# Kernel tuning notes

Measured on AMD Instinct MI355X. Metric: run time of the kernel, lower is better.

## Reference

```python
import jax, jax.numpy as jnp
import numpy as np

N, H, L, O = 8192, 512, 3, 512
LN_EPS = 1e-5


def setup_inputs() -> dict:
    key = jax.random.key(0)
    ks = jax.random.split(key, 8)
    # sparse symmetric adjacency with positive weights, zero diagonal
    u = jax.random.uniform(ks[0], (N, N))
    w = jax.random.uniform(ks[1], (N, N)) * 0.9 + 0.1
    A = jnp.where(u < 0.004, w, 0.0)
    A = (A + A.T) * 0.5
    A = A * (1.0 - jnp.eye(N, dtype=A.dtype))
    s = 0.02
    return {
        "node_feat": jax.random.normal(ks[2], (1, N, H), jnp.float32),
        "adj": A[None],
        "conv_w": jax.random.normal(ks[3], (L, H, H), jnp.float32) * s,
        "conv_b": jnp.zeros((L, H), jnp.float32),
        "mlp_w": jax.random.normal(ks[4], (L, H, H), jnp.float32) * s,
        "mlp_b": jnp.zeros((L, H), jnp.float32),
        "ln_g": jnp.ones((L, H), jnp.float32),
        "ln_b": jnp.zeros((L, H), jnp.float32),
        "lin_w": jax.random.normal(ks[5], (H, O), jnp.float32) * s,
        "lin_b": jnp.zeros((O,), jnp.float32),
    }


def _layer_norm(x, g, b):
    mu = jnp.mean(x, axis=-1, keepdims=True)
    var = jnp.mean(jnp.square(x - mu), axis=-1, keepdims=True)
    return (x - mu) * jax.lax.rsqrt(var + LN_EPS) * g + b


def reference(node_feat, adj, conv_w, conv_b, mlp_w, mlp_b, ln_g, ln_b, lin_w, lin_b):
    x = node_feat[0]          # [N, H]
    A = adj[0]                # [N, N]
    A = jnp.where(A > 0, A, 0.0)  # edges are positive entries only
    # gcn_norm: add self-loops (weight 1) only where missing
    d = jnp.diagonal(A)
    A1 = A + jnp.diag(jnp.where(d > 0, 0.0, 1.0))
    # deg scattered at target (edge_index[1] = column)
    deg = jnp.sum(A1, axis=0)
    dinv = jnp.where(deg > 0, deg ** -0.5, 0.0)
    Ahat = dinv[:, None] * A1 * dinv[None, :]  # [N, N]
    for l in range(L):
        # GCNConv: linear, propagate (aggregate at col), bias
        x = Ahat.T @ (x @ conv_w[l]) + conv_b[l]
        # MLP: Linear -> LayerNorm -> ReLU
        x = jax.nn.relu(_layer_norm(x @ mlp_w[l] + mlp_b[l], ln_g[l], ln_b[l]))
    mu = (x @ lin_w + lin_b)[None]  # [1, N, O]
    return mu
```

## Files before the change

### kernel.cpp

```cpp
#include <hip/hip_runtime.h>

#define NN 8192
#define HD 512
#define NL 3
#define CAP 128
#define LN_EPS 1e-5f

typedef _Float16 f16;
typedef _Float16 f16x8 __attribute__((ext_vector_type(8)));
typedef _Float16 f16x4 __attribute__((ext_vector_type(4)));
typedef _Float16 f16x2 __attribute__((ext_vector_type(2)));
typedef float f32x4 __attribute__((ext_vector_type(4)));

__device__ __forceinline__ unsigned short f16_bits(f16 h) {
  union { f16 h; unsigned short u; } x; x.h = h; return x.u;
}
__device__ __forceinline__ f16 bits_f16(unsigned short u) {
  union { unsigned short u; f16 h; } x; x.u = u; return x.h;
}

__global__ __launch_bounds__(256) void k_prep(const float* __restrict__ A,
                                              const float* __restrict__ x0,
                                              unsigned* __restrict__ ell,
                                              int* __restrict__ nnz8,
                                              float* __restrict__ dinv,
                                              f16* __restrict__ xs) {
  __shared__ int wtot[4];
  __shared__ float wsum[4];
  __shared__ float sdinv;
  const int r = blockIdx.x;
  const int t = threadIdx.x;
  const int lane = t & 63;
  const int wv = t >> 6;
  const float4* ar = (const float4*)(A + (size_t)r * NN);
  unsigned* er = ell + (size_t)r * CAP;

  float4 v[8];
  int c = 0;
  float s = 0.f;
  #pragma unroll
  for (int i = 0; i < 8; i++) {
    v[i] = ar[t + i * 256];
    c += (v[i].x > 0.f) + (v[i].y > 0.f) + (v[i].z > 0.f) + (v[i].w > 0.f);
    s += v[i].x + v[i].y + v[i].z + v[i].w;
  }
  int inc = c;
  #pragma unroll
  for (int d = 1; d < 64; d <<= 1) {
    int vv = __shfl_up(inc, d);
    if (lane >= d) inc += vv;
  }
  float ss = s;
  #pragma unroll
  for (int m = 1; m < 64; m <<= 1) ss += __shfl_xor(ss, m);
  if (lane == 63) wtot[wv] = inc;
  if (lane == 0) wsum[wv] = ss;
  __syncthreads();
  int base = inc - c;
  for (int w = 0; w < wv; w++) base += wtot[w];

  int o = base;
  #pragma unroll
  for (int i = 0; i < 8; i++) {
    float vals[4] = {v[i].x, v[i].y, v[i].z, v[i].w};
    #pragma unroll
    for (int q = 0; q < 4; q++) {
      float val = vals[q];
      if (val > 0.f) {
        if (o < CAP) er[o] = ((unsigned)f16_bits((f16)val) << 16) | (unsigned)((t + i * 256) * 4 + q);
        o++;
      }
    }
  }
  if (t == 255) {
    int ne = wtot[0] + wtot[1] + wtot[2] + wtot[3];
    if (ne < CAP) er[ne] = (0x3C00u << 16) | (unsigned)r;
    int ne1 = ne + 1; if (ne1 > CAP) ne1 = CAP;
    int n8 = (ne1 + 7) & ~7;
    for (int k = ne1; k < n8; k++) er[k] = (unsigned)r;
    nnz8[r] = n8;
    float deg = wsum[0] + wsum[1] + wsum[2] + wsum[3] + 1.f;
    float di = rsqrtf(deg);
    dinv[r] = di;
    sdinv = di;
  }
  __syncthreads();
  {
    const float di = sdinv;
    const float2 xv = ((const float2*)(x0 + (size_t)r * HD))[t];
    f16x2 o2 = {(f16)(xv.x * di), (f16)(xv.y * di)};
    ((f16x2*)(xs + (size_t)r * HD))[t] = o2;
  }
}

__global__ __launch_bounds__(256) void k_spmm(const unsigned* __restrict__ ell,
                                              const int* __restrict__ nnz8,
                                              const float* __restrict__ dinv,
                                              const f16* __restrict__ xs,
                                              f16* __restrict__ y) {
  const int bid = blockIdx.x;
  const int chunk = bid >> 11;
  const int rb = bid & 2047;
  const int r = __builtin_amdgcn_readfirstlane(rb * 4 + (threadIdx.x >> 6));
  const int lane = threadIdx.x & 63;
  const int c0 = chunk * 128 + lane * 2;
  const uint4* er = (const uint4*)(ell + (size_t)r * CAP);
  const int ne = nnz8[r];
  const f16* xc = xs + c0;
  float a0 = 0.f, a1 = 0.f;
  for (int e8 = 0; e8 < (ne >> 3); e8++) {
    const uint4 ea = er[e8 * 2];
    const uint4 eb = er[e8 * 2 + 1];
    unsigned wv[8] = {ea.x, ea.y, ea.z, ea.w, eb.x, eb.y, eb.z, eb.w};
    f16x2 xv[8];
    #pragma unroll
    for (int q = 0; q < 8; q++)
      xv[q] = *(const f16x2*)(xc + (size_t)(wv[q] & 0xFFFFu) * HD);
    #pragma unroll
    for (int q = 0; q < 8; q++) {
      const float fw = (float)bits_f16((unsigned short)(wv[q] >> 16));
      a0 = fmaf(fw, (float)xv[q][0], a0);
      a1 = fmaf(fw, (float)xv[q][1], a1);
    }
  }
  const float s = dinv[r];
  f16x2 o = {(f16)(a0 * s), (f16)(a1 * s)};
  *(f16x2*)(y + (size_t)r * HD + c0) = o;
}

__global__ __launch_bounds__(512) void k_gemm_ln(const f16* __restrict__ y,
                                                 const f16* __restrict__ WT,
                                                 const float* __restrict__ bias,
                                                 const float* __restrict__ g,
                                                 const float* __restrict__ bb,
                                                 const float* __restrict__ dscale,
                                                 f16* __restrict__ outp) {
  __shared__ float red[32][4][2];
  const int t = threadIdx.x;
  const int lane = t & 63;
  const int w = t >> 6;
  const int wm = w >> 2;
  const int wn = w & 3;
  const int m0 = blockIdx.x * 32;
  const int rl = lane & 15, kg = (lane >> 4) * 8;
  const f16* aP = y + (size_t)(m0 + wm * 16 + rl) * HD + kg;
  const f16* bP = WT + (size_t)(wn * 128 + rl) * HD + kg;

  f32x4 acc[8];
  #pragma unroll
  for (int j = 0; j < 8; j++) { f32x4 z = {0.f, 0.f, 0.f, 0.f}; acc[j] = z; }

  #pragma unroll 2
  for (int ks = 0; ks < HD; ks += 32) {
    const f16x8 af = *(const f16x8*)(aP + ks);
    #pragma unroll
    for (int j = 0; j < 8; j++) {
      const f16x8 bf = *(const f16x8*)(bP + (size_t)j * 16 * HD + ks);
      acc[j] = __builtin_amdgcn_mfma_f32_16x16x32_f16(af, bf, acc[j], 0, 0, 0);
    }
  }

  const int cg = lane >> 4, cl = lane & 15;
  float av[8][4];
  #pragma unroll
  for (int j = 0; j < 8; j++) {
    const float bv = bias[wn * 128 + j * 16 + cl];
    #pragma unroll
    for (int r = 0; r < 4; r++) av[j][r] = acc[j][r] + bv;
  }
  #pragma unroll
  for (int r = 0; r < 4; r++) {
    float s = 0.f, sq = 0.f;
    #pragma unroll
    for (int j = 0; j < 8; j++) { s += av[j][r]; sq += av[j][r] * av[j][r]; }
    #pragma unroll
    for (int m = 1; m < 16; m <<= 1) { s += __shfl_xor(s, m); sq += __shfl_xor(sq, m); }
    if (cl == 0) {
      red[wm * 16 + cg * 4 + r][wn][0] = s;
      red[wm * 16 + cg * 4 + r][wn][1] = sq;
    }
  }
  __syncthreads();
  #pragma unroll
  for (int r = 0; r < 4; r++) {
    const int rb = wm * 16 + cg * 4 + r;
    float s = 0.f, sq = 0.f;
    #pragma unroll
    for (int q = 0; q < 4; q++) { s += red[rb][q][0]; sq += red[rb][q][1]; }
    const float mu = s * (1.f / HD);
    const float rs = rsqrtf(sq * (1.f / HD) - mu * mu + LN_EPS);
    const int row = m0 + rb;
    const float dsc = dscale ? dscale[row] : 1.f;
    #pragma unroll
    for (int j = 0; j < 8; j++) {
      const int col = wn * 128 + j * 16 + cl;
      const float val = fmaxf((av[j][r] - mu) * rs * g[col] + bb[col], 0.f) * dsc;
      outp[(size_t)row * HD + col] = (f16)val;
    }
  }
}

__global__ __launch_bounds__(256) void k_gemm_direct(const f16* __restrict__ A,
                                                     const f16* __restrict__ BT,
                                                     float* __restrict__ C,
                                                     const float* __restrict__ bias) {
  const int t = threadIdx.x;
  const int lane = t & 63;
  const int wave = t >> 6;
  const int wm = wave >> 1, wn = wave & 1;
  const int m0 = blockIdx.x * 128, n0 = blockIdx.y * 128;
  const int rl = lane & 15, kg = (lane >> 4) * 8;

  const f16* aP[4];
  const f16* bP[4];
  #pragma unroll
  for (int i = 0; i < 4; i++)
    aP[i] = A + (size_t)(m0 + wm * 64 + i * 16 + rl) * HD + kg;
  #pragma unroll
  for (int j = 0; j < 4; j++)
    bP[j] = BT + (size_t)(n0 + wn * 64 + j * 16 + rl) * HD + kg;

  f32x4 acc[4][4];
  #pragma unroll
  for (int i = 0; i < 4; i++)
    #pragma unroll
    for (int j = 0; j < 4; j++) {
      f32x4 z = {0.f, 0.f, 0.f, 0.f};
      acc[i][j] = z;
    }

  #pragma unroll 4
  for (int ks = 0; ks < HD; ks += 32) {
    f16x8 af[4], bf[4];
    #pragma unroll
    for (int i = 0; i < 4; i++) af[i] = *(const f16x8*)(aP[i] + ks);
    #pragma unroll
    for (int j = 0; j < 4; j++) bf[j] = *(const f16x8*)(bP[j] + ks);
    #pragma unroll
    for (int i = 0; i < 4; i++)
      #pragma unroll
      for (int j = 0; j < 4; j++)
        acc[i][j] = __builtin_amdgcn_mfma_f32_16x16x32_f16(af[i], bf[j], acc[i][j], 0, 0, 0);
  }

  const int cg = lane >> 4, cl = lane & 15;
  #pragma unroll
  for (int i = 0; i < 4; i++) {
    #pragma unroll
    for (int j = 0; j < 4; j++) {
      const int col = n0 + wn * 64 + j * 16 + cl;
      const float bv = bias ? bias[col] : 0.f;
      #pragma unroll
      for (int rr = 0; rr < 4; rr++) {
        const int row = m0 + wm * 64 + i * 16 + cg * 4 + rr;
        C[(size_t)row * HD + col] = acc[i][j][rr] + bv;
      }
    }
  }
}

__global__ __launch_bounds__(256) void k_weights(const float* __restrict__ convw,
                                                 const float* __restrict__ mlpw,
                                                 const float* __restrict__ convb,
                                                 const float* __restrict__ mlpb,
                                                 const float* __restrict__ lw,
                                                 f16* __restrict__ WlT,
                                                 float* __restrict__ bl,
                                                 f16* __restrict__ lwT) {
  const int l = blockIdx.y;
  const int bx = blockIdx.x;
  const int t = threadIdx.x;
  if (bx < 256) {
    const int m0 = bx * 2;
    const float* Wc = convw + (size_t)l * HD * HD;
    const float* Wm = mlpw + (size_t)l * HD * HD;
    f16* o = WlT + (size_t)l * HD * HD;
    float a00 = 0.f, a01 = 0.f, a10 = 0.f, a11 = 0.f;
    const float* wc0 = Wc + (size_t)m0 * HD;
    const float* wc1 = Wc + (size_t)(m0 + 1) * HD;
    for (int k = 0; k < HD; k++) {
      const float w0 = Wm[(size_t)k * HD + t];
      const float w1 = Wm[(size_t)k * HD + t + 256];
      const float c0 = wc0[k];
      const float c1 = wc1[k];
      a00 = fmaf(c0, w0, a00);
      a01 = fmaf(c0, w1, a01);
      a10 = fmaf(c1, w0, a10);
      a11 = fmaf(c1, w1, a11);
    }
    o[(size_t)t * HD + m0] = (f16)a00;
    o[(size_t)(t + 256) * HD + m0] = (f16)a01;
    o[(size_t)t * HD + m0 + 1] = (f16)a10;
    o[(size_t)(t + 256) * HD + m0 + 1] = (f16)a11;
  } else if (bx == 256) {
    const float* Wm = mlpw + (size_t)l * HD * HD;
    float acc0 = mlpb[l * HD + t];
    float acc1 = mlpb[l * HD + t + 256];
    for (int k = 0; k < HD; k++) {
      const float cb = convb[l * HD + k];
      acc0 = fmaf(cb, Wm[(size_t)k * HD + t], acc0);
      acc1 = fmaf(cb, Wm[(size_t)k * HD + t + 256], acc1);
    }
    bl[l * HD + t] = acc0;
    bl[l * HD + t + 256] = acc1;
  } else if (l == 0) {
    const int base = (bx - 257) * 16384;
    #pragma unroll 4
    for (int j = 0; j < 64; j++) {
      const int idx = base + j * 256 + t;
      const int k = idx >> 9, n = idx & 511;
      lwT[(size_t)n * HD + k] = (f16)lw[idx];
    }
  }
}

extern "C" void kernel_launch(void* const* d_in, const int* in_sizes, int n_in,
                              void* d_out, int out_size, void* d_ws, size_t ws_size,
                              hipStream_t stream) {
  const float* node_feat = (const float*)d_in[0];
  const float* adj       = (const float*)d_in[1];
  const float* conv_w    = (const float*)d_in[2];
  const float* conv_b    = (const float*)d_in[3];
  const float* mlp_w     = (const float*)d_in[4];
  const float* mlp_b     = (const float*)d_in[5];
  const float* ln_g      = (const float*)d_in[6];
  const float* ln_b      = (const float*)d_in[7];
  const float* lin_w     = (const float*)d_in[8];
  const float* lin_b     = (const float*)d_in[9];
  float* out = (float*)d_out;

  char* p = (char*)d_ws;
  unsigned* ell = (unsigned*)p; p += (size_t)NN * CAP * 4;
  int* nnz8  = (int*)p;   p += (size_t)NN * 4;
  float* dinv = (float*)p; p += (size_t)NN * 4;
  f16* xsA   = (f16*)p;   p += (size_t)NN * HD * 2;
  f16* xsB   = (f16*)p;   p += (size_t)NN * HD * 2;
  f16* ybuf  = (f16*)p;   p += (size_t)NN * HD * 2;
  f16* WlT   = (f16*)p;   p += (size_t)NL * HD * HD * 2;
  f16* lwT   = (f16*)p;   p += (size_t)HD * HD * 2;
  float* bl  = (float*)p; p += (size_t)NL * HD * 4;

  k_prep<<<NN, 256, 0, stream>>>(adj, node_feat, ell, nnz8, dinv, xsA);
  k_weights<<<dim3(273, NL), 256, 0, stream>>>(conv_w, mlp_w, conv_b, mlp_b,
                                               lin_w, WlT, bl, lwT);

  f16* xcur = xsA;
  for (int l = 0; l < NL; l++) {
    k_spmm<<<NN, 256, 0, stream>>>(ell, nnz8, dinv, xcur, ybuf);
    f16* nxt = (xcur == xsA) ? xsB : xsA;
    k_gemm_ln<<<NN / 32, 512, 0, stream>>>(ybuf, WlT + (size_t)l * HD * HD,
                                           bl + l * HD, ln_g + l * HD, ln_b + l * HD,
                                           (l < 2) ? dinv : nullptr, nxt);
    xcur = nxt;
  }
  k_gemm_direct<<<dim3(64, 4), 256, 0, stream>>>(xcur, lwT, out, lin_b);
}
```

Baseline: 337.6 us.

## Fuse sparse aggregation into GEMM+LayerNorm kernel and merge weight prep into prep

The separate SpMM kernel is folded into the per-layer GEMM+LayerNorm kernel. Each block aggregates its 32 rows into a swizzled LDS tile and then runs the MFMA GEMM from LDS, which removes the global round-trip through the y buffer and three kernel launches. Weight folding is also merged into k_prep as extra blocks, dropping one more launch. The cost is that only 256 blocks do the gather (versus 8192 before), with each wave handling 4 rows serially using 16-byte loads, so latency hiding for the gather may suffer.

```diff
diff --git a/kernel.cpp b/kernel.cpp
--- a/kernel.cpp
+++ b/kernel.cpp
@@ -21,15 +21,74 @@
 
 __global__ __launch_bounds__(256) void k_prep(const float* __restrict__ A,
                                               const float* __restrict__ x0,
+                                              const float* __restrict__ convw,
+                                              const float* __restrict__ mlpw,
+                                              const float* __restrict__ convb,
+                                              const float* __restrict__ mlpb,
+                                              const float* __restrict__ lw,
                                               unsigned* __restrict__ ell,
                                               int* __restrict__ nnz8,
                                               float* __restrict__ dinv,
-                                              f16* __restrict__ xs) {
+                                              f16* __restrict__ xs,
+                                              f16* __restrict__ WlT,
+                                              float* __restrict__ bl,
+                                              f16* __restrict__ lwT) {
+  const int b = blockIdx.x;
+  const int t = threadIdx.x;
+
+  if (b >= NN) {
+    const int wl = b - NN;
+    const int l = wl / 273;
+    const int bx = wl % 273;
+    if (bx < 256) {
+      const int m0 = bx * 2;
+      const float* Wc = convw + (size_t)l * HD * HD;
+      const float* Wm = mlpw + (size_t)l * HD * HD;
+      f16* o = WlT + (size_t)l * HD * HD;
+      float a00 = 0.f, a01 = 0.f, a10 = 0.f, a11 = 0.f;
+      const float* wc0 = Wc + (size_t)m0 * HD;
+      const float* wc1 = Wc + (size_t)(m0 + 1) * HD;
+      for (int k = 0; k < HD; k++) {
+        const float w0 = Wm[(size_t)k * HD + t];
+        const float w1 = Wm[(size_t)k * HD + t + 256];
+        const float c0 = wc0[k];
+        const float c1 = wc1[k];
+        a00 = fmaf(c0, w0, a00);
+        a01 = fmaf(c0, w1, a01);
+        a10 = fmaf(c1, w0, a10);
+        a11 = fmaf(c1, w1, a11);
+      }
+      o[(size_t)t * HD + m0] = (f16)a00;
+      o[(size_t)(t + 256) * HD + m0] = (f16)a01;
+      o[(size_t)t * HD + m0 + 1] = (f16)a10;
+      o[(size_t)(t + 256) * HD + m0 + 1] = (f16)a11;
+    } else if (bx == 256) {
+      const float* Wm = mlpw + (size_t)l * HD * HD;
+      float acc0 = mlpb[l * HD + t];
+      float acc1 = mlpb[l * HD + t + 256];
+      for (int k = 0; k < HD; k++) {
+        const float cb = convb[l * HD + k];
+        acc0 = fmaf(cb, Wm[(size_t)k * HD + t], acc0);
+        acc1 = fmaf(cb, Wm[(size_t)k * HD + t + 256], acc1);
+      }
+      bl[l * HD + t] = acc0;
+      bl[l * HD + t + 256] = acc1;
+    } else if (l == 0) {
+      const int base = (bx - 257) * 16384;
+      #pragma unroll 4
+      for (int j = 0; j < 64; j++) {
+        const int idx = base + j * 256 + t;
+        const int k = idx >> 9, n = idx & 511;
+        lwT[(size_t)n * HD + k] = (f16)lw[idx];
+      }
+    }
+    return;
+  }
+
   __shared__ int wtot[4];
   __shared__ float wsum[4];
   __shared__ float sdinv;
-  const int r = blockIdx.x;
-  const int t = threadIdx.x;
+  const int r = b;
   const int lane = t & 63;
   const int wv = t >> 6;
   const float4* ar = (const float4*)(A + (size_t)r * NN);
@@ -93,58 +152,62 @@
   }
 }
 
-__global__ __launch_bounds__(256) void k_spmm(const unsigned* __restrict__ ell,
-                                              const int* __restrict__ nnz8,
-                                              const float* __restrict__ dinv,
-                                              const f16* __restrict__ xs,
-                                              f16* __restrict__ y) {
-  const int bid = blockIdx.x;
-  const int chunk = bid >> 11;
-  const int rb = bid & 2047;
-  const int r = __builtin_amdgcn_readfirstlane(rb * 4 + (threadIdx.x >> 6));
-  const int lane = threadIdx.x & 63;
-  const int c0 = chunk * 128 + lane * 2;
-  const uint4* er = (const uint4*)(ell + (size_t)r * CAP);
-  const int ne = nnz8[r];
-  const f16* xc = xs + c0;
-  float a0 = 0.f, a1 = 0.f;
-  for (int e8 = 0; e8 < (ne >> 3); e8++) {
-    const uint4 ea = er[e8 * 2];
-    const uint4 eb = er[e8 * 2 + 1];
-    unsigned wv[8] = {ea.x, ea.y, ea.z, ea.w, eb.x, eb.y, eb.z, eb.w};
-    f16x2 xv[8];
-    #pragma unroll
-    for (int q = 0; q < 8; q++)
-      xv[q] = *(const f16x2*)(xc + (size_t)(wv[q] & 0xFFFFu) * HD);
-    #pragma unroll
-    for (int q = 0; q < 8; q++) {
-      const float fw = (float)bits_f16((unsigned short)(wv[q] >> 16));
-      a0 = fmaf(fw, (float)xv[q][0], a0);
-      a1 = fmaf(fw, (float)xv[q][1], a1);
-    }
-  }
-  const float s = dinv[r];
-  f16x2 o = {(f16)(a0 * s), (f16)(a1 * s)};
-  *(f16x2*)(y + (size_t)r * HD + c0) = o;
-}
-
-__global__ __launch_bounds__(512) void k_gemm_ln(const f16* __restrict__ y,
-                                                 const f16* __restrict__ WT,
-                                                 const float* __restrict__ bias,
-                                                 const float* __restrict__ g,
-                                                 const float* __restrict__ bb,
-                                                 const float* __restrict__ dscale,
-                                                 f16* __restrict__ outp) {
+__global__ __launch_bounds__(512) void k_layer(const unsigned* __restrict__ ell,
+                                               const int* __restrict__ nnz8,
+                                               const float* __restrict__ dinv,
+                                               const f16* __restrict__ xs,
+                                               const f16* __restrict__ WT,
+                                               const float* __restrict__ bias,
+                                               const float* __restrict__ g,
+                                               const float* __restrict__ bb,
+                                               const float* __restrict__ dscale,
+                                               f16* __restrict__ outp) {
+  __shared__ __attribute__((aligned(16))) f16 ylds[32 * HD];
   __shared__ float red[32][4][2];
   const int t = threadIdx.x;
   const int lane = t & 63;
   const int w = t >> 6;
+  const int m0 = blockIdx.x * 32;
+
+  {
+    const int wu = __builtin_amdgcn_readfirstlane(w);
+    for (int i = 0; i < 4; i++) {
+      const int r = m0 + wu * 4 + i;
+      const uint4* er = (const uint4*)(ell + (size_t)r * CAP);
+      const int ne = nnz8[r];
+      float acc[8] = {0.f, 0.f, 0.f, 0.f, 0.f, 0.f, 0.f, 0.f};
+      for (int e8 = 0; e8 < (ne >> 3); e8++) {
+        const uint4 ea = er[e8 * 2];
+        const uint4 eb = er[e8 * 2 + 1];
+        unsigned wvs[8] = {ea.x, ea.y, ea.z, ea.w, eb.x, eb.y, eb.z, eb.w};
+        f16x8 xv[8];
+        #pragma unroll
+        for (int q = 0; q < 8; q++)
+          xv[q] = *(const f16x8*)(xs + (size_t)(wvs[q] & 0xFFFFu) * HD + lane * 8);
+        #pragma unroll
+        for (int q = 0; q < 8; q++) {
+          const float fw = (float)bits_f16((unsigned short)(wvs[q] >> 16));
+          #pragma unroll
+          for (int j = 0; j < 8; j++)
+            acc[j] = fmaf(fw, (float)xv[q][j], acc[j]);
+        }
+      }
+      const float s = dinv[r];
+      f16x8 o;
+      #pragma unroll
+      for (int j = 0; j < 8; j++) o[j] = (f16)(acc[j] * s);
+      const int lr = wu * 4 + i;
+      const int ce = (lane * 8) ^ ((lr & 7) << 3);
+      *(f16x8*)(&ylds[lr * HD + ce]) = o;
+    }
+  }
+  __syncthreads();
+
   const int wm = w >> 2;
   const int wn = w & 3;
-  const int m0 = blockIdx.x * 32;
-  const int rl = lane & 15, kg = (lane >> 4) * 8;
-  const f16* aP = y + (size_t)(m0 + wm * 16 + rl) * HD + kg;
-  const f16* bP = WT + (size_t)(wn * 128 + rl) * HD + kg;
+  const int rl = lane & 15, kghi = lane >> 4;
+  const int lr = wm * 16 + rl;
+  const f16* bP = WT + (size_t)(wn * 128 + rl) * HD + kghi * 8;
 
   f32x4 acc[8];
   #pragma unroll
@@ -152,7 +215,8 @@
 
   #pragma unroll 2
   for (int ks = 0; ks < HD; ks += 32) {
-    const f16x8 af = *(const f16x8*)(aP + ks);
+    const int ce = (ks + kghi * 8) ^ ((lr & 7) << 3);
+    const f16x8 af = *(const f16x8*)(&ylds[lr * HD + ce]);
     #pragma unroll
     for (int j = 0; j < 8; j++) {
       const f16x8 bf = *(const f16x8*)(bP + (size_t)j * 16 * HD + ks);
@@ -160,7 +224,7 @@
     }
   }
 
-  const int cg = lane >> 4, cl = lane & 15;
+  const int cg = kghi, cl = rl;
   float av[8][4];
   #pragma unroll
   for (int j = 0; j < 8; j++) {
@@ -255,61 +319,6 @@
         const int row = m0 + wm * 64 + i * 16 + cg * 4 + rr;
         C[(size_t)row * HD + col] = acc[i][j][rr] + bv;
       }
-    }
-  }
-}
-
-__global__ __launch_bounds__(256) void k_weights(const float* __restrict__ convw,
-                                                 const float* __restrict__ mlpw,
-                                                 const float* __restrict__ convb,
-                                                 const float* __restrict__ mlpb,
-                                                 const float* __restrict__ lw,
-                                                 f16* __restrict__ WlT,
-                                                 float* __restrict__ bl,
-                                                 f16* __restrict__ lwT) {
-  const int l = blockIdx.y;
-  const int bx = blockIdx.x;
-  const int t = threadIdx.x;
-  if (bx < 256) {
-    const int m0 = bx * 2;
-    const float* Wc = convw + (size_t)l * HD * HD;
-    const float* Wm = mlpw + (size_t)l * HD * HD;
-    f16* o = WlT + (size_t)l * HD * HD;
-    float a00 = 0.f, a01 = 0.f, a10 = 0.f, a11 = 0.f;
-    const float* wc0 = Wc + (size_t)m0 * HD;
-    const float* wc1 = Wc + (size_t)(m0 + 1) * HD;
-    for (int k = 0; k < HD; k++) {
-      const float w0 = Wm[(size_t)k * HD + t];
-      const float w1 = Wm[(size_t)k * HD + t + 256];
-      const float c0 = wc0[k];
-      const float c1 = wc1[k];
-      a00 = fmaf(c0, w0, a00);
-      a01 = fmaf(c0, w1, a01);
-      a10 = fmaf(c1, w0, a10);
-      a11 = fmaf(c1, w1, a11);
-    }
-    o[(size_t)t * HD + m0] = (f16)a00;
-    o[(size_t)(t + 256) * HD + m0] = (f16)a01;
-    o[(size_t)t * HD + m0 + 1] = (f16)a10;
-    o[(size_t)(t + 256) * HD + m0 + 1] = (f16)a11;
-  } else if (bx == 256) {
-    const float* Wm = mlpw + (size_t)l * HD * HD;
-    float acc0 = mlpb[l * HD + t];
-    float acc1 = mlpb[l * HD + t + 256];
-    for (int k = 0; k < HD; k++) {
-      const float cb = convb[l * HD + k];
-      acc0 = fmaf(cb, Wm[(size_t)k * HD + t], acc0);
-      acc1 = fmaf(cb, Wm[(size_t)k * HD + t + 256], acc1);
-    }
-    bl[l * HD + t] = acc0;
-    bl[l * HD + t + 256] = acc1;
-  } else if (l == 0) {
-    const int base = (bx - 257) * 16384;
-    #pragma unroll 4
-    for (int j = 0; j < 64; j++) {
-      const int idx = base + j * 256 + t;
-      const int k = idx >> 9, n = idx & 511;
-      lwT[(size_t)n * HD + k] = (f16)lw[idx];
     }
   }
 }
@@ -335,22 +344,21 @@
   float* dinv = (float*)p; p += (size_t)NN * 4;
   f16* xsA   = (f16*)p;   p += (size_t)NN * HD * 2;
   f16* xsB   = (f16*)p;   p += (size_t)NN * HD * 2;
-  f16* ybuf  = (f16*)p;   p += (size_t)NN * HD * 2;
   f16* WlT   = (f16*)p;   p += (size_t)NL * HD * HD * 2;
   f16* lwT   = (f16*)p;   p += (size_t)HD * HD * 2;
   float* bl  = (float*)p; p += (size_t)NL * HD * 4;
 
-  k_prep<<<NN, 256, 0, stream>>>(adj, node_feat, ell, nnz8, dinv, xsA);
-  k_weights<<<dim3(273, NL), 256, 0, stream>>>(conv_w, mlp_w, conv_b, mlp_b,
-                                               lin_w, WlT, bl, lwT);
+  k_prep<<<NN + 273 * NL, 256, 0, stream>>>(adj, node_feat, conv_w, mlp_w,
+                                            conv_b, mlp_b, lin_w,
+                                            ell, nnz8, dinv, xsA, WlT, bl, lwT);
 
   f16* xcur = xsA;
   for (int l = 0; l < NL; l++) {
-    k_spmm<<<NN, 256, 0, stream>>>(ell, nnz8, dinv, xcur, ybuf);
     f16* nxt = (xcur == xsA) ? xsB : xsA;
-    k_gemm_ln<<<NN / 32, 512, 0, stream>>>(ybuf, WlT + (size_t)l * HD * HD,
-                                           bl + l * HD, ln_g + l * HD, ln_b + l * HD,
-                                           (l < 2) ? dinv : nullptr, nxt);
+    k_layer<<<NN / 32, 512, 0, stream>>>(ell, nnz8, dinv, xcur,
+                                         WlT + (size_t)l * HD * HD, bl + l * HD,
+                                         ln_g + l * HD, ln_b + l * HD,
+                                         (l < 2) ? dinv : nullptr, nxt);
     xcur = nxt;
   }
   k_gemm_direct<<<dim3(64, 4), 256, 0, stream>>>(xcur, lwT, out, lin_b);
```

New measurement: 350.9 us. 1.04x slower.

## Fuse weight prep into adjacency prep kernel, rotate row reads, interleave spmm chunks

Applied to the files above, without the earlier changes.

Merges the weight-folding kernel into the adjacency preprocessing kernel as extra leading blocks, removing one launch and letting weight work overlap the adjacency scan. The adjacency row scan no longer keeps the row in registers; it reads the row twice (count pass, then emit pass) with a per-row rotated start offset, to spread concurrent row accesses across memory channels and to lower register pressure. The SpMM block mapping now puts the four column chunks of a row group in adjacent block ids, which should improve cache reuse of the ELL rows. The cost is a second read of each adjacency row, which may hit in cache or add HBM traffic, and ELL entries within a row are no longer in column order.

```diff
diff --git a/kernel.cpp b/kernel.cpp
--- a/kernel.cpp
+++ b/kernel.cpp
@@ -4,6 +4,7 @@
 #define HD 512
 #define NL 3
 #define CAP 128
+#define NWB (273 * NL)
 #define LN_EPS 1e-5f
 
 typedef _Float16 f16;
@@ -21,28 +22,87 @@
 
 __global__ __launch_bounds__(256) void k_prep(const float* __restrict__ A,
                                               const float* __restrict__ x0,
+                                              const float* __restrict__ convw,
+                                              const float* __restrict__ mlpw,
+                                              const float* __restrict__ convb,
+                                              const float* __restrict__ mlpb,
+                                              const float* __restrict__ lw,
                                               unsigned* __restrict__ ell,
                                               int* __restrict__ nnz8,
                                               float* __restrict__ dinv,
-                                              f16* __restrict__ xs) {
+                                              f16* __restrict__ xs,
+                                              f16* __restrict__ WlT,
+                                              float* __restrict__ bl,
+                                              f16* __restrict__ lwT) {
+  const int b = blockIdx.x;
+  const int t = threadIdx.x;
+
+  if (b < NWB) {
+    const int l = b / 273;
+    const int bx = b % 273;
+    if (bx < 256) {
+      const int m0 = bx * 2;
+      const float* Wc = convw + (size_t)l * HD * HD;
+      const float* Wm = mlpw + (size_t)l * HD * HD;
+      f16* o = WlT + (size_t)l * HD * HD;
+      float a00 = 0.f, a01 = 0.f, a10 = 0.f, a11 = 0.f;
+      const float* wc0 = Wc + (size_t)m0 * HD;
+      const float* wc1 = Wc + (size_t)(m0 + 1) * HD;
+      for (int k = 0; k < HD; k++) {
+        const float w0 = Wm[(size_t)k * HD + t];
+        const float w1 = Wm[(size_t)k * HD + t + 256];
+        const float c0 = wc0[k];
+        const float c1 = wc1[k];
+        a00 = fmaf(c0, w0, a00);
+        a01 = fmaf(c0, w1, a01);
+        a10 = fmaf(c1, w0, a10);
+        a11 = fmaf(c1, w1, a11);
+      }
+      o[(size_t)t * HD + m0] = (f16)a00;
+      o[(size_t)(t + 256) * HD + m0] = (f16)a01;
+      o[(size_t)t * HD + m0 + 1] = (f16)a10;
+      o[(size_t)(t + 256) * HD + m0 + 1] = (f16)a11;
+    } else if (bx == 256) {
+      const float* Wm = mlpw + (size_t)l * HD * HD;
+      float acc0 = mlpb[l * HD + t];
+      float acc1 = mlpb[l * HD + t + 256];
+      for (int k = 0; k < HD; k++) {
+        const float cb = convb[l * HD + k];
+        acc0 = fmaf(cb, Wm[(size_t)k * HD + t], acc0);
+        acc1 = fmaf(cb, Wm[(size_t)k * HD + t + 256], acc1);
+      }
+      bl[l * HD + t] = acc0;
+      bl[l * HD + t + 256] = acc1;
+    } else if (l == 0) {
+      const int base = (bx - 257) * 16384;
+      #pragma unroll 4
+      for (int j = 0; j < 64; j++) {
+        const int idx = base + j * 256 + t;
+        const int k = idx >> 9, n = idx & 511;
+        lwT[(size_t)n * HD + k] = (f16)lw[idx];
+      }
+    }
+    return;
+  }
+
   __shared__ int wtot[4];
   __shared__ float wsum[4];
   __shared__ float sdinv;
-  const int r = blockIdx.x;
-  const int t = threadIdx.x;
+  const int r = b - NWB;
   const int lane = t & 63;
   const int wv = t >> 6;
   const float4* ar = (const float4*)(A + (size_t)r * NN);
   unsigned* er = ell + (size_t)r * CAP;
-
-  float4 v[8];
+  const int rot = (r * 5) & 2047;
+
   int c = 0;
   float s = 0.f;
   #pragma unroll
   for (int i = 0; i < 8; i++) {
-    v[i] = ar[t + i * 256];
-    c += (v[i].x > 0.f) + (v[i].y > 0.f) + (v[i].z > 0.f) + (v[i].w > 0.f);
-    s += v[i].x + v[i].y + v[i].z + v[i].w;
+    const int f = (t + i * 256 + rot) & 2047;
+    const float4 v = ar[f];
+    c += (v.x > 0.f) + (v.y > 0.f) + (v.z > 0.f) + (v.w > 0.f);
+    s += v.x + v.y + v.z + v.w;
   }
   int inc = c;
   #pragma unroll
@@ -62,12 +122,14 @@
   int o = base;
   #pragma unroll
   for (int i = 0; i < 8; i++) {
-    float vals[4] = {v[i].x, v[i].y, v[i].z, v[i].w};
+    const int f = (t + i * 256 + rot) & 2047;
+    const float4 v = ar[f];
+    float vals[4] = {v.x, v.y, v.z, v.w};
     #pragma unroll
     for (int q = 0; q < 4; q++) {
       float val = vals[q];
       if (val > 0.f) {
-        if (o < CAP) er[o] = ((unsigned)f16_bits((f16)val) << 16) | (unsigned)((t + i * 256) * 4 + q);
+        if (o < CAP) er[o] = ((unsigned)f16_bits((f16)val) << 16) | (unsigned)(f * 4 + q);
         o++;
       }
     }
@@ -99,8 +161,8 @@
                                               const f16* __restrict__ xs,
                                               f16* __restrict__ y) {
   const int bid = blockIdx.x;
-  const int chunk = bid >> 11;
-  const int rb = bid & 2047;
+  const int chunk = bid & 3;
+  const int rb = bid >> 2;
   const int r = __builtin_amdgcn_readfirstlane(rb * 4 + (threadIdx.x >> 6));
   const int lane = threadIdx.x & 63;
   const int c0 = chunk * 128 + lane * 2;
@@ -259,61 +321,6 @@
   }
 }
 
-__global__ __launch_bounds__(256) void k_weights(const float* __restrict__ convw,
-                                                 const float* __restrict__ mlpw,
-                                                 const float* __restrict__ convb,
-                                                 const float* __restrict__ mlpb,
-                                                 const float* __restrict__ lw,
-                                                 f16* __restrict__ WlT,
-                                                 float* __restrict__ bl,
-                                                 f16* __restrict__ lwT) {
-  const int l = blockIdx.y;
-  const int bx = blockIdx.x;
-  const int t = threadIdx.x;
-  if (bx < 256) {
-    const int m0 = bx * 2;
-    const float* Wc = convw + (size_t)l * HD * HD;
-    const float* Wm = mlpw + (size_t)l * HD * HD;
-    f16* o = WlT + (size_t)l * HD * HD;
-    float a00 = 0.f, a01 = 0.f, a10 = 0.f, a11 = 0.f;
-    const float* wc0 = Wc + (size_t)m0 * HD;
-    const float* wc1 = Wc + (size_t)(m0 + 1) * HD;
-    for (int k = 0; k < HD; k++) {
-      const float w0 = Wm[(size_t)k * HD + t];
-      const float w1 = Wm[(size_t)k * HD + t + 256];
-      const float c0 = wc0[k];
-      const float c1 = wc1[k];
-      a00 = fmaf(c0, w0, a00);
-      a01 = fmaf(c0, w1, a01);
-      a10 = fmaf(c1, w0, a10);
-      a11 = fmaf(c1, w1, a11);
-    }
-    o[(size_t)t * HD + m0] = (f16)a00;
-    o[(size_t)(t + 256) * HD + m0] = (f16)a01;
-    o[(size_t)t * HD + m0 + 1] = (f16)a10;
-    o[(size_t)(t + 256) * HD + m0 + 1] = (f16)a11;
-  } else if (bx == 256) {
-    const float* Wm = mlpw + (size_t)l * HD * HD;
-    float acc0 = mlpb[l * HD + t];
-    float acc1 = mlpb[l * HD + t + 256];
-    for (int k = 0; k < HD; k++) {
-      const float cb = convb[l * HD + k];
-      acc0 = fmaf(cb, Wm[(size_t)k * HD + t], acc0);
-      acc1 = fmaf(cb, Wm[(size_t)k * HD + t + 256], acc1);
-    }
-    bl[l * HD + t] = acc0;
-    bl[l * HD + t + 256] = acc1;
-  } else if (l == 0) {
-    const int base = (bx - 257) * 16384;
-    #pragma unroll 4
-    for (int j = 0; j < 64; j++) {
-      const int idx = base + j * 256 + t;
-      const int k = idx >> 9, n = idx & 511;
-      lwT[(size_t)n * HD + k] = (f16)lw[idx];
-    }
-  }
-}
-
 extern "C" void kernel_launch(void* const* d_in, const int* in_sizes, int n_in,
                               void* d_out, int out_size, void* d_ws, size_t ws_size,
                               hipStream_t stream) {
@@ -340,9 +347,9 @@
   f16* lwT   = (f16*)p;   p += (size_t)HD * HD * 2;
   float* bl  = (float*)p; p += (size_t)NL * HD * 4;
 
-  k_prep<<<NN, 256, 0, stream>>>(adj, node_feat, ell, nnz8, dinv, xsA);
-  k_weights<<<dim3(273, NL), 256, 0, stream>>>(conv_w, mlp_w, conv_b, mlp_b,
-                                               lin_w, WlT, bl, lwT);
+  k_prep<<<NWB + NN, 256, 0, stream>>>(adj, node_feat, conv_w, mlp_w,
+                                       conv_b, mlp_b, lin_w,
+                                       ell, nnz8, dinv, xsA, WlT, bl, lwT);
 
   f16* xcur = xsA;
   for (int l = 0; l < NL; l++) {
```

Measured after the change: 332.5 us. Within noise of the previous version (-1.5%).
